# Optimization experiments

Measured on AMD Instinct MI355X. Metric: run time of the kernel, lower is better.

Reference implementation:

```python
import jax, jax.numpy as jnp
import numpy as np

D_MODEL = 2048
N_HEADS = 16
N_KV = 8
HEAD_DIM = 128
G = N_HEADS // N_KV  # q heads per kv head
SCALE = float(np.sqrt(HEAD_DIM))
B, T = 2, 2048


def setup_inputs() -> dict:
    key = jax.random.key(0)
    k1, k2, k3, k4, k5 = jax.random.split(key, 5)
    s = 0.02
    return {
        "x": jax.random.normal(k1, (B, T, D_MODEL), dtype=jnp.float32),
        "Wq": jax.random.normal(k2, (N_HEADS * HEAD_DIM, D_MODEL), dtype=jnp.float32) * s,
        "Wk": jax.random.normal(k3, (N_KV * HEAD_DIM, D_MODEL), dtype=jnp.float32) * s,
        "Wv": jax.random.normal(k4, (N_KV * HEAD_DIM, D_MODEL), dtype=jnp.float32) * s,
        "Wo": jax.random.normal(k5, (D_MODEL, N_HEADS * HEAD_DIM), dtype=jnp.float32) * s,
    }


def reference(x, Wq, Wk, Wv, Wo):
    # Projections (nn.Linear: y = x @ W.T), dropout prob = 0 so omitted.
    b, t, _ = x.shape
    q = (x @ Wq.T).reshape(b, t, N_KV, G, HEAD_DIM)   # (B,T,Hkv,G,d)
    k = (x @ Wk.T).reshape(b, t, N_KV, HEAD_DIM)      # (B,T,Hkv,d)
    v = (x @ Wv.T).reshape(b, t, N_KV, HEAD_DIM)
    # GQA: each kv head shared by G query heads (equivalent to repeat_interleave).
    scores = jnp.einsum('btghd,bsgd->bghts', q, k) / SCALE  # (B,Hkv,G,T,T)
    attn = jax.nn.softmax(scores, axis=-1)
    out = jnp.einsum('bghts,bsgd->btghd', attn, v)          # (B,T,Hkv,G,d)
    out = out.reshape(b, t, N_HEADS * HEAD_DIM)
    return out @ Wo.T
```

## Files before the change

kernel.cpp:

```cpp
#include <hip/hip_runtime.h>
#include <hip/hip_bf16.h>

typedef __attribute__((ext_vector_type(8))) short short8;
typedef __attribute__((ext_vector_type(4))) float floatx4;

__device__ inline unsigned short f2bf(float f) {
    unsigned int u = __float_as_uint(f);
    u += 0x7fffu + ((u >> 16) & 1u);
    return (unsigned short)(u >> 16);
}

__device__ inline unsigned int pk_bf16(float lo, float hi) {
    __hip_bfloat162 h = __float22bfloat162_rn(float2{lo, hi});
    unsigned int u;
    __builtin_memcpy(&u, &h, 4);
    return u;
}

__global__ void cast_all_kernel(const float* __restrict__ x,
                                const float* __restrict__ wq,
                                const float* __restrict__ wk,
                                const float* __restrict__ wv,
                                const float* __restrict__ wo,
                                unsigned short* __restrict__ xb,
                                unsigned short* __restrict__ wqkb,
                                unsigned short* __restrict__ wvb,
                                unsigned short* __restrict__ wob) {
    const float C2 = 0.08838834764831845f * 1.4426950408889634f;
    int bid = blockIdx.x;
    const float* src;
    unsigned short* dst;
    int base;
    float sc = 1.0f;
    if (bid < 8192)       { src = x;  dst = xb;             base = bid; }
    else if (bid < 12288) { src = wq; dst = wqkb;           base = bid - 8192; sc = C2; }
    else if (bid < 14336) { src = wk; dst = wqkb + 4194304; base = bid - 12288; }
    else if (bid < 16384) { src = wv; dst = wvb;            base = bid - 14336; }
    else                  { src = wo; dst = wob;            base = bid - 16384; }
    int i = base * 256 + threadIdx.x;
    float4 v = ((const float4*)src)[i];
    ushort4 o;
    o.x = f2bf(v.x * sc); o.y = f2bf(v.y * sc);
    o.z = f2bf(v.z * sc); o.w = f2bf(v.w * sc);
    ((ushort4*)dst)[i] = o;
}

template <int OUT_BF16>
__device__ __forceinline__ void gemm256_body(
        const unsigned short* __restrict__ A,
        const unsigned short* __restrict__ B,
        void* __restrict__ Cp, int ldc, int m0, int n0,
        unsigned short* sL) {
    const int tid  = threadIdx.x;
    const int wave = tid >> 6;
    const int lane = tid & 63;
    const int l16  = lane & 15;
    const int lq   = lane >> 4;
    const int wm   = (wave >> 2) * 128;
    const int wn   = (wave & 3) * 64;
    const int kx   = lq ^ (l16 & 3);

    floatx4 acc[8][4] = {};

    const unsigned short* gA[2];
    const unsigned short* gB[2];
#pragma unroll
    for (int i = 0; i < 2; i++) {
        int c   = wave * 2 + i;
        int row = c * 16 + (lane >> 2);
        int g   = (lane & 3) ^ (row & 3);
        gA[i] = A + (size_t)(m0 + row) * 2048 + g * 8;
        gB[i] = B + (size_t)(n0 + row) * 2048 + g * 8;
    }

#define STG_A32(slot)                                                          \
    do {                                                                       \
        _Pragma("unroll")                                                      \
        for (int i = 0; i < 2; i++) {                                          \
            __builtin_amdgcn_global_load_lds(                                  \
                (const __attribute__((address_space(1))) void*)gA[i],          \
                (__attribute__((address_space(3))) void*)(sL + (slot) * 16384 +\
                                                          (wave * 2 + i) * 512),\
                16, 0, 0);                                                     \
            gA[i] += 32;                                                       \
        }                                                                      \
    } while (0)
#define STG_B32(slot)                                                          \
    do {                                                                       \
        _Pragma("unroll")                                                      \
        for (int i = 0; i < 2; i++) {                                          \
            __builtin_amdgcn_global_load_lds(                                  \
                (const __attribute__((address_space(1))) void*)gB[i],          \
                (__attribute__((address_space(3))) void*)(sL + (slot) * 16384 +\
                                                  8192 + (wave * 2 + i) * 512),\
                16, 0, 0);                                                     \
            gB[i] += 32;                                                       \
        }                                                                      \
    } while (0)

    STG_A32(0); STG_B32(0);
    STG_A32(1); STG_B32(1);

    for (int t = 0; t < 64; t++) {
        const int sc = t & 3;
        const int sn = (t + 2) & 3;
        if (t < 63) asm volatile("s_waitcnt vmcnt(4)" ::: "memory");
        else        asm volatile("s_waitcnt vmcnt(0)" ::: "memory");
        __builtin_amdgcn_s_barrier();
        asm volatile("" ::: "memory");

        const unsigned short* sAc = sL + sc * 16384;
        const unsigned short* sBc = sAc + 8192;
        short8 af[4], bf[4];

#pragma unroll
        for (int mb = 0; mb < 4; mb++)
            af[mb] = *(const short8*)(sAc + (wm + mb * 16 + l16) * 32 + kx * 8);
#pragma unroll
        for (int nb = 0; nb < 4; nb++)
            bf[nb] = *(const short8*)(sBc + (wn + nb * 16 + l16) * 32 + kx * 8);
        if (t < 62) STG_A32(sn);
        __builtin_amdgcn_s_barrier();
        asm volatile("s_waitcnt lgkmcnt(0)" ::: "memory");
        __builtin_amdgcn_sched_barrier(0);
        __builtin_amdgcn_s_setprio(1);
#pragma unroll
        for (int mb = 0; mb < 4; mb++)
#pragma unroll
            for (int nb = 0; nb < 4; nb++)
                acc[mb][nb] = __builtin_amdgcn_mfma_f32_16x16x32_bf16(
                    af[mb], bf[nb], acc[mb][nb], 0, 0, 0);
        __builtin_amdgcn_s_setprio(0);
        __builtin_amdgcn_s_barrier();
        asm volatile("" ::: "memory");

#pragma unroll
        for (int mb = 0; mb < 4; mb++)
            af[mb] = *(const short8*)(sAc + (wm + 64 + mb * 16 + l16) * 32 + kx * 8);
        if (t < 62) STG_B32(sn);
        __builtin_amdgcn_s_barrier();
        asm volatile("s_waitcnt lgkmcnt(0)" ::: "memory");
        __builtin_amdgcn_sched_barrier(0);
        __builtin_amdgcn_s_setprio(1);
#pragma unroll
        for (int mb = 0; mb < 4; mb++)
#pragma unroll
            for (int nb = 0; nb < 4; nb++)
                acc[4 + mb][nb] = __builtin_amdgcn_mfma_f32_16x16x32_bf16(
                    af[mb], bf[nb], acc[4 + mb][nb], 0, 0, 0);
        __builtin_amdgcn_s_setprio(0);
    }
#undef STG_A32
#undef STG_B32

#pragma unroll
    for (int mb = 0; mb < 8; mb++)
#pragma unroll
        for (int nb = 0; nb < 4; nb++)
#pragma unroll
            for (int r = 0; r < 4; r++) {
                int row = m0 + wm + mb * 16 + lq * 4 + r;
                int col = n0 + wn + nb * 16 + l16;
                if (OUT_BF16)
                    ((unsigned short*)Cp)[(size_t)row * ldc + col] = f2bf(acc[mb][nb][r]);
                else
                    ((float*)Cp)[(size_t)row * ldc + col] = acc[mb][nb][r];
            }
}

template <int OUT_BF16>
__device__ __forceinline__ void gemm128_body(
        const unsigned short* __restrict__ A,
        const unsigned short* __restrict__ B,
        void* __restrict__ Cp, int ldc, int m0, int n0,
        unsigned short* sL) {
    const int tid  = threadIdx.x;
    const int wave = tid >> 6;
    const int lane = tid & 63;
    const int l16  = lane & 15;
    const int lq   = lane >> 4;
    const int wm   = (wave >> 2) * 64;
    const int wn   = (wave & 3) * 64;
    const int kx   = lq ^ (l16 & 3);

    floatx4 acc[4][4] = {};

    const unsigned short* gA0;
    const unsigned short* gB[2];
    {
        int row = wave * 16 + (lane >> 2);
        int g   = (lane & 3) ^ (row & 3);
        gA0 = A + (size_t)(m0 + row) * 2048 + g * 8;
    }
#pragma unroll
    for (int i = 0; i < 2; i++) {
        int c   = wave * 2 + i;
        int row = c * 16 + (lane >> 2);
        int g   = (lane & 3) ^ (row & 3);
        gB[i] = B + (size_t)(n0 + row) * 2048 + g * 8;
    }

#define STG_O(slot)                                                            \
    do {                                                                       \
        __builtin_amdgcn_global_load_lds(                                      \
            (const __attribute__((address_space(1))) void*)gA0,                \
            (__attribute__((address_space(3))) void*)(sL + (slot) * 12288 +    \
                                                      wave * 512),             \
            16, 0, 0);                                                         \
        gA0 += 32;                                                             \
        _Pragma("unroll")                                                      \
        for (int i = 0; i < 2; i++) {                                          \
            __builtin_amdgcn_global_load_lds(                                  \
                (const __attribute__((address_space(1))) void*)gB[i],          \
                (__attribute__((address_space(3))) void*)(sL + (slot) * 12288 +\
                                                  4096 + (wave * 2 + i) * 512),\
                16, 0, 0);                                                     \
            gB[i] += 32;                                                       \
        }                                                                      \
    } while (0)

    STG_O(0); STG_O(1);

    for (int t = 0; t < 64; t++) {
        const int sc = t & 3;
        const int sn = (t + 2) & 3;
        if (t < 63) asm volatile("s_waitcnt vmcnt(3)" ::: "memory");
        else        asm volatile("s_waitcnt vmcnt(0)" ::: "memory");
        __builtin_amdgcn_s_barrier();
        asm volatile("" ::: "memory");

        const unsigned short* sAc = sL + sc * 12288;
        const unsigned short* sBc = sAc + 4096;
        short8 af[4], bf[4];
#pragma unroll
        for (int mb = 0; mb < 4; mb++)
            af[mb] = *(const short8*)(sAc + (wm + mb * 16 + l16) * 32 + kx * 8);
#pragma unroll
        for (int nb = 0; nb < 4; nb++)
            bf[nb] = *(const short8*)(sBc + (wn + nb * 16 + l16) * 32 + kx * 8);
        if (t < 62) STG_O(sn);
        __builtin_amdgcn_s_barrier();
        asm volatile("s_waitcnt lgkmcnt(0)" ::: "memory");
        __builtin_amdgcn_sched_barrier(0);
        __builtin_amdgcn_s_setprio(1);
#pragma unroll
        for (int mb = 0; mb < 4; mb++)
#pragma unroll
            for (int nb = 0; nb < 4; nb++)
                acc[mb][nb] = __builtin_amdgcn_mfma_f32_16x16x32_bf16(
                    af[mb], bf[nb], acc[mb][nb], 0, 0, 0);
        __builtin_amdgcn_s_setprio(0);
    }
#undef STG_O

#pragma unroll
    for (int mb = 0; mb < 4; mb++)
#pragma unroll
        for (int nb = 0; nb < 4; nb++)
#pragma unroll
            for (int r = 0; r < 4; r++) {
                int row = m0 + wm + mb * 16 + lq * 4 + r;
                int col = n0 + wn + nb * 16 + l16;
                if (OUT_BF16)
                    ((unsigned short*)Cp)[(size_t)row * ldc + col] = f2bf(acc[mb][nb][r]);
                else
                    ((float*)Cp)[(size_t)row * ldc + col] = acc[mb][nb][r];
            }
}

__global__ __launch_bounds__(512, 1) void gemm_qkv_kernel(
        const unsigned short* __restrict__ x_bf,
        const unsigned short* __restrict__ Wqk,
        const unsigned short* __restrict__ Wv,
        unsigned short* __restrict__ QKb,
        unsigned short* __restrict__ Vtb) {
    __shared__ __align__(16) unsigned short sL[4 * 16384];
    const int bid = blockIdx.x;
    if (bid < 192) {
        gemm256_body<1>(x_bf, Wqk, QKb, 3072,
                        (bid / 12) * 256, (bid % 12) * 256, sL);
    } else {
        int t = bid - 192;
        gemm256_body<1>(Wv, x_bf, Vtb, 4096,
                        (t / 16) * 256, (t % 16) * 256, sL);
    }
}

__global__ __launch_bounds__(512, 1) void gemm_o_kernel(
        const unsigned short* __restrict__ A,
        const unsigned short* __restrict__ B,
        float* __restrict__ C) {
    __shared__ __align__(16) unsigned short sL[4 * 12288];
    gemm128_body<0>(A, B, C, 2048,
                    blockIdx.y * 128, blockIdx.x * 256, sL);
}

__global__ __launch_bounds__(256, 2) void flash_kernel(
        const unsigned short* __restrict__ QK,
        const unsigned short* __restrict__ Vt,
        unsigned short* __restrict__ O) {
    __shared__ __align__(16) unsigned short smem[40960];

    const int tid  = threadIdx.x;
    const int wave = tid >> 6;
    const int lane = tid & 63;
    const int l16  = lane & 15;
    const int lq   = lane >> 4;
    const int qt   = blockIdx.x;
    const int bh   = blockIdx.y;
    const int b    = bh >> 4;
    const int h    = bh & 15;
    const int kvh  = h >> 1;
    const size_t tokbase = (size_t)b * 2048 + qt * 128 + wave * 32;

    short8 qf[2][4];
#pragma unroll
    for (int qb = 0; qb < 2; qb++) {
        const unsigned short* qp =
            QK + (tokbase + qb * 16 + l16) * 3072 + h * 128 + lq * 8;
#pragma unroll
        for (int c = 0; c < 4; c++) qf[qb][c] = *(const short8*)(qp + c * 32);
    }

    const unsigned short* gKe =
        QK + ((size_t)b * 2048 + wave * 16 + lq) * 3072 + 2048 + kvh * 128 +
        (l16 ^ lq) * 8;
    const unsigned short* gKo =
        QK + ((size_t)b * 2048 + wave * 16 + 4 + lq) * 3072 + 2048 + kvh * 128 +
        (l16 ^ (lq + 4)) * 8;
    const unsigned short* gV0 =
        Vt + (size_t)(kvh * 128 + wave * 32 + (lane >> 3)) * 4096 +
        (size_t)b * 2048 + ((lane & 7) ^ (lane >> 3)) * 8;

#define STAGE_KT(sKd, sVd)                                                     \
    do {                                                                       \
        _Pragma("unroll")                                                      \
        for (int i = 0; i < 4; i++) {                                          \
            const unsigned short* gk =                                         \
                ((i & 1) ? gKo : gKe) + (i >> 1) * 24576;                      \
            __builtin_amdgcn_global_load_lds(                                  \
                (const __attribute__((address_space(1))) void*)gk,             \
                (__attribute__((address_space(3))) void*)((sKd) +              \
                                                          (wave * 4 + i) * 512),\
                16, 0, 0);                                                     \
            __builtin_amdgcn_global_load_lds(                                  \
                (const __attribute__((address_space(1))) void*)(gV0 +          \
                                                               i * 32768),     \
                (__attribute__((address_space(3))) void*)((sVd) +              \
                                                          (wave * 4 + i) * 512),\
                16, 0, 0);                                                     \
        }                                                                      \
        gKe += 196608; gKo += 196608; gV0 += 64;                               \
    } while (0)

    unsigned short* pB = smem + 32768 + wave * 2048;

    floatx4 oacc[2][8] = {};
    float l_run[2] = {0.0f, 0.0f};

    STAGE_KT(smem, smem + 16384);
    asm volatile("s_waitcnt vmcnt(0)" ::: "memory");
    __builtin_amdgcn_s_barrier();
    asm volatile("" ::: "memory");

    for (int kt = 0; kt < 32; kt++) {
        const int cur = kt & 1;
        const unsigned short* sKc = smem + cur * 8192;
        const unsigned short* sVc = smem + 16384 + cur * 8192;
        if (kt < 31) {
            unsigned short* sKn = smem + (cur ^ 1) * 8192;
            unsigned short* sVn = smem + 16384 + (cur ^ 1) * 8192;
            STAGE_KT(sKn, sVn);
        }

#pragma unroll
        for (int kb = 0; kb < 2; kb++) {
            floatx4 sacc[2] = {};
#pragma unroll
            for (int c = 0; c < 4; c++) {
                short8 kf = *(const short8*)(
                    sKc + (kb * 16 + l16) * 128 + (((c * 4 + lq) ^ (l16 & 7)) * 8));
#pragma unroll
                for (int qb = 0; qb < 2; qb++)
                    sacc[qb] = __builtin_amdgcn_mfma_f32_16x16x32_bf16(
                        kf, qf[qb][c], sacc[qb], 0, 0, 0);
            }
#pragma unroll
            for (int qb = 0; qb < 2; qb++) {
                float p0 = __builtin_exp2f(sacc[qb][0]);
                float p1 = __builtin_exp2f(sacc[qb][1]);
                float p2 = __builtin_exp2f(sacc[qb][2]);
                float p3 = __builtin_exp2f(sacc[qb][3]);
                l_run[qb] += (p0 + p1) + (p2 + p3);
                int row = qb * 16 + l16;
                uint2 u;
                u.x = pk_bf16(p0, p1);
                u.y = pk_bf16(p2, p3);
                *(uint2*)(pB + row * 64 +
                          (((kb * 2 + (lq >> 1)) ^ (row & 7)) * 8) +
                          (lq & 1) * 4) = u;
            }
        }
        asm volatile("s_waitcnt lgkmcnt(0)" ::: "memory");

        short8 pf0[2];
#pragma unroll
        for (int qb = 0; qb < 2; qb++) {
            int row = qb * 16 + l16;
            pf0[qb] = *(const short8*)(pB + row * 64 +
                                       ((lq ^ (row & 7)) * 8));
        }

        __builtin_amdgcn_s_setprio(1);
#pragma unroll
        for (int nb = 0; nb < 8; nb++) {
            short8 vf = *(const short8*)(
                sVc + (nb * 16 + l16) * 64 + ((lq ^ (l16 & 7)) * 8));
#pragma unroll
            for (int qb = 0; qb < 2; qb++)
                oacc[qb][nb] = __builtin_amdgcn_mfma_f32_16x16x32_bf16(
                    vf, pf0[qb], oacc[qb][nb], 0, 0, 0);
        }
        __builtin_amdgcn_s_setprio(0);

#pragma unroll
        for (int kb = 2; kb < 4; kb++) {
            floatx4 sacc[2] = {};
#pragma unroll
            for (int c = 0; c < 4; c++) {
                short8 kf = *(const short8*)(
                    sKc + (kb * 16 + l16) * 128 + (((c * 4 + lq) ^ (l16 & 7)) * 8));
#pragma unroll
                for (int qb = 0; qb < 2; qb++)
                    sacc[qb] = __builtin_amdgcn_mfma_f32_16x16x32_bf16(
                        kf, qf[qb][c], sacc[qb], 0, 0, 0);
            }
#pragma unroll
            for (int qb = 0; qb < 2; qb++) {
                float p0 = __builtin_exp2f(sacc[qb][0]);
                float p1 = __builtin_exp2f(sacc[qb][1]);
                float p2 = __builtin_exp2f(sacc[qb][2]);
                float p3 = __builtin_exp2f(sacc[qb][3]);
                l_run[qb] += (p0 + p1) + (p2 + p3);
                int row = qb * 16 + l16;
                uint2 u;
                u.x = pk_bf16(p0, p1);
                u.y = pk_bf16(p2, p3);
                *(uint2*)(pB + row * 64 +
                          (((kb * 2 + (lq >> 1)) ^ (row & 7)) * 8) +
                          (lq & 1) * 4) = u;
            }
        }
        asm volatile("s_waitcnt lgkmcnt(0)" ::: "memory");

        short8 pf1[2];
#pragma unroll
        for (int qb = 0; qb < 2; qb++) {
            int row = qb * 16 + l16;
            pf1[qb] = *(const short8*)(pB + row * 64 +
                                       (((4 + lq) ^ (row & 7)) * 8));
        }

        __builtin_amdgcn_s_setprio(1);
#pragma unroll
        for (int nb = 0; nb < 8; nb++) {
            short8 vf = *(const short8*)(
                sVc + (nb * 16 + l16) * 64 + (((4 + lq) ^ (l16 & 7)) * 8));
#pragma unroll
            for (int qb = 0; qb < 2; qb++)
                oacc[qb][nb] = __builtin_amdgcn_mfma_f32_16x16x32_bf16(
                    vf, pf1[qb], oacc[qb][nb], 0, 0, 0);
        }
        __builtin_amdgcn_s_setprio(0);

        asm volatile("s_waitcnt vmcnt(0)" ::: "memory");
        __builtin_amdgcn_s_barrier();
        asm volatile("" ::: "memory");
    }
#undef STAGE_KT

#pragma unroll
    for (int qb = 0; qb < 2; qb++) {
        float l = l_run[qb];
        l += __shfl_xor(l, 16);
        l += __shfl_xor(l, 32);
        float inv = 1.0f / l;
        size_t row = (tokbase + qb * 16 + l16) * 2048 + h * 128;
#pragma unroll
        for (int nb = 0; nb < 8; nb++) {
            uint2 u;
            u.x = pk_bf16(oacc[qb][nb][0] * inv, oacc[qb][nb][1] * inv);
            u.y = pk_bf16(oacc[qb][nb][2] * inv, oacc[qb][nb][3] * inv);
            *(uint2*)(O + row + nb * 16 + lq * 4) = u;
        }
    }
}

extern "C" void kernel_launch(void* const* d_in, const int* in_sizes, int n_in,
                              void* d_out, int out_size, void* d_ws, size_t ws_size,
                              hipStream_t stream) {
    const float* x  = (const float*)d_in[0];
    const float* Wq = (const float*)d_in[1];
    const float* Wk = (const float*)d_in[2];
    const float* Wv = (const float*)d_in[3];
    const float* Wo = (const float*)d_in[4];

    char* ws = (char*)d_ws;
    unsigned short* x_bf   = (unsigned short*)(ws);
    unsigned short* Wqk_bf = (unsigned short*)(ws + 16777216);
    unsigned short* Wv_bf  = (unsigned short*)(ws + 29360128);
    unsigned short* Wo_bf  = (unsigned short*)(ws + 33554432);
    unsigned short* QKb    = (unsigned short*)(ws + 41943040);
    unsigned short* Vtb    = (unsigned short*)(ws + 67108864);
    unsigned short* Ob     = (unsigned short*)(ws + 75497472);

    cast_all_kernel<<<dim3(20480), 256, 0, stream>>>(
        x, Wq, Wk, Wv, Wo, x_bf, Wqk_bf, Wv_bf, Wo_bf);

    gemm_qkv_kernel<<<dim3(256), 512, 0, stream>>>(x_bf, Wqk_bf, Wv_bf, QKb, Vtb);

    flash_kernel<<<dim3(16, 32), 256, 0, stream>>>(QKb, Vtb, Ob);

    gemm_o_kernel<<<dim3(8, 32), 512, 0, stream>>>(Ob, Wo_bf, (float*)d_out);
}
```

Measured before the change: 310.7 us.

## Single-buffer K/V in flash kernel to fit three blocks per CU

Replaces the double-buffered K/V LDS tiles with single buffers, shrinking shared memory from 80KB to 48KB and raising launch bounds to 3 blocks per CU. K is reloaded after its last use mid-iteration and V after the second PV pass, each guarded by extra barriers. The goal is higher occupancy to hide latency, at the cost of losing prefetch overlap within a block: V's load now waits with vmcnt(0) at iteration end, with added barriers and possible register pressure from the tighter bound.

```diff
diff --git a/kernel.cpp b/kernel.cpp
--- a/kernel.cpp
+++ b/kernel.cpp
@@ -295,11 +295,11 @@
                     blockIdx.y * 128, blockIdx.x * 256, sL);
 }
 
-__global__ __launch_bounds__(256, 2) void flash_kernel(
+__global__ __launch_bounds__(256, 3) void flash_kernel(
         const unsigned short* __restrict__ QK,
         const unsigned short* __restrict__ Vt,
         unsigned short* __restrict__ O) {
-    __shared__ __align__(16) unsigned short smem[40960];
+    __shared__ __align__(16) unsigned short smem[24576];
 
     const int tid  = threadIdx.x;
     const int wave = tid >> 6;
@@ -332,7 +332,10 @@
         Vt + (size_t)(kvh * 128 + wave * 32 + (lane >> 3)) * 4096 +
         (size_t)b * 2048 + ((lane & 7) ^ (lane >> 3)) * 8;
 
-#define STAGE_KT(sKd, sVd)                                                     \
+    unsigned short* sK = smem;
+    unsigned short* sV = smem + 8192;
+
+#define STAGE_K()                                                              \
     do {                                                                       \
         _Pragma("unroll")                                                      \
         for (int i = 0; i < 4; i++) {                                          \
@@ -340,46 +343,45 @@
                 ((i & 1) ? gKo : gKe) + (i >> 1) * 24576;                      \
             __builtin_amdgcn_global_load_lds(                                  \
                 (const __attribute__((address_space(1))) void*)gk,             \
-                (__attribute__((address_space(3))) void*)((sKd) +              \
+                (__attribute__((address_space(3))) void*)(sK +                 \
                                                           (wave * 4 + i) * 512),\
                 16, 0, 0);                                                     \
+        }                                                                      \
+        gKe += 196608; gKo += 196608;                                          \
+    } while (0)
+#define STAGE_V()                                                              \
+    do {                                                                       \
+        _Pragma("unroll")                                                      \
+        for (int i = 0; i < 4; i++) {                                          \
             __builtin_amdgcn_global_load_lds(                                  \
                 (const __attribute__((address_space(1))) void*)(gV0 +          \
                                                                i * 32768),     \
-                (__attribute__((address_space(3))) void*)((sVd) +              \
+                (__attribute__((address_space(3))) void*)(sV +                 \
                                                           (wave * 4 + i) * 512),\
                 16, 0, 0);                                                     \
         }                                                                      \
-        gKe += 196608; gKo += 196608; gV0 += 64;                               \
+        gV0 += 64;                                                             \
     } while (0)
 
-    unsigned short* pB = smem + 32768 + wave * 2048;
+    unsigned short* pB = smem + 16384 + wave * 2048;
 
     floatx4 oacc[2][8] = {};
     float l_run[2] = {0.0f, 0.0f};
 
-    STAGE_KT(smem, smem + 16384);
+    STAGE_K();
+    STAGE_V();
     asm volatile("s_waitcnt vmcnt(0)" ::: "memory");
     __builtin_amdgcn_s_barrier();
     asm volatile("" ::: "memory");
 
     for (int kt = 0; kt < 32; kt++) {
-        const int cur = kt & 1;
-        const unsigned short* sKc = smem + cur * 8192;
-        const unsigned short* sVc = smem + 16384 + cur * 8192;
-        if (kt < 31) {
-            unsigned short* sKn = smem + (cur ^ 1) * 8192;
-            unsigned short* sVn = smem + 16384 + (cur ^ 1) * 8192;
-            STAGE_KT(sKn, sVn);
-        }
-
 #pragma unroll
         for (int kb = 0; kb < 2; kb++) {
             floatx4 sacc[2] = {};
 #pragma unroll
             for (int c = 0; c < 4; c++) {
                 short8 kf = *(const short8*)(
-                    sKc + (kb * 16 + l16) * 128 + (((c * 4 + lq) ^ (l16 & 7)) * 8));
+                    sK + (kb * 16 + l16) * 128 + (((c * 4 + lq) ^ (l16 & 7)) * 8));
 #pragma unroll
                 for (int qb = 0; qb < 2; qb++)
                     sacc[qb] = __builtin_amdgcn_mfma_f32_16x16x32_bf16(
@@ -415,7 +417,7 @@
 #pragma unroll
         for (int nb = 0; nb < 8; nb++) {
             short8 vf = *(const short8*)(
-                sVc + (nb * 16 + l16) * 64 + ((lq ^ (l16 & 7)) * 8));
+                sV + (nb * 16 + l16) * 64 + ((lq ^ (l16 & 7)) * 8));
 #pragma unroll
             for (int qb = 0; qb < 2; qb++)
                 oacc[qb][nb] = __builtin_amdgcn_mfma_f32_16x16x32_bf16(
@@ -429,7 +431,7 @@
 #pragma unroll
             for (int c = 0; c < 4; c++) {
                 short8 kf = *(const short8*)(
-                    sKc + (kb * 16 + l16) * 128 + (((c * 4 + lq) ^ (l16 & 7)) * 8));
+                    sK + (kb * 16 + l16) * 128 + (((c * 4 + lq) ^ (l16 & 7)) * 8));
 #pragma unroll
                 for (int qb = 0; qb < 2; qb++)
                     sacc[qb] = __builtin_amdgcn_mfma_f32_16x16x32_bf16(
@@ -453,6 +455,10 @@
         }
         asm volatile("s_waitcnt lgkmcnt(0)" ::: "memory");
 
+        __builtin_amdgcn_s_barrier();
+        asm volatile("" ::: "memory");
+        if (kt < 31) STAGE_K();
+
         short8 pf1[2];
 #pragma unroll
         for (int qb = 0; qb < 2; qb++) {
@@ -465,7 +471,7 @@
 #pragma unroll
         for (int nb = 0; nb < 8; nb++) {
             short8 vf = *(const short8*)(
-                sVc + (nb * 16 + l16) * 64 + (((4 + lq) ^ (l16 & 7)) * 8));
+                sV + (nb * 16 + l16) * 64 + (((4 + lq) ^ (l16 & 7)) * 8));
 #pragma unroll
             for (int qb = 0; qb < 2; qb++)
                 oacc[qb][nb] = __builtin_amdgcn_mfma_f32_16x16x32_bf16(
@@ -473,11 +479,17 @@
         }
         __builtin_amdgcn_s_setprio(0);
 
+        asm volatile("s_waitcnt lgkmcnt(0)" ::: "memory");
+        __builtin_amdgcn_s_barrier();
+        asm volatile("" ::: "memory");
+        if (kt < 31) STAGE_V();
+
         asm volatile("s_waitcnt vmcnt(0)" ::: "memory");
         __builtin_amdgcn_s_barrier();
         asm volatile("" ::: "memory");
     }
-#undef STAGE_KT
+#undef STAGE_K
+#undef STAGE_V
 
 #pragma unroll
     for (int qb = 0; qb < 2; qb++) {
```

Result: slower. 342.7 us (+10.3%).
